# Kernel optimization log

Hardware: AMD Instinct MI355X
Metric: run time of the kernel (lower is better)

The kernel has to match this reference:

```python
import jax, jax.numpy as jnp
import numpy as np

B, L, V, E, H, DOUT = 32, 128, 30000, 300, 512, 5
NUM_STEPS = 5
WINDOW = 1


def setup_inputs() -> dict:
    key = jax.random.key(0)
    ks = jax.random.split(key, 16)
    def p(k, shape, scale=0.02):
        return jax.random.normal(k, shape, jnp.float32) * scale
    tokens = jax.random.randint(ks[0], (B, L), 1, V)
    lengths = jnp.maximum(jax.random.randint(ks[1], (B,), 1, L + 1), 8)
    embed = p(ks[2], (V, E), 0.1).at[0].set(0.0)  # padding_idx=0 row zeroed
    W0 = p(ks[3], (E, H)); b0 = jnp.zeros((H,), jnp.float32)
    Wg = p(ks[4], (3 * H + E + H, 7 * H)); bg = jnp.zeros((7 * H,), jnp.float32)
    Wgf = p(ks[5], (2 * H, H)); bgf = jnp.zeros((H,), jnp.float32)
    Wfi = p(ks[6], (2 * H, H)); bfi = jnp.zeros((H,), jnp.float32)
    Wgo = p(ks[7], (2 * H, H)); bgo = jnp.zeros((H,), jnp.float32)
    W1 = p(ks[8], (H, 2 * H)); b1 = jnp.zeros((2 * H,), jnp.float32)
    W2 = p(ks[9], (2 * H, DOUT)); b2 = jnp.zeros((DOUT,), jnp.float32)
    return dict(tokens=tokens, lengths=lengths, embed=embed, W0=W0, b0=b0,
                Wg=Wg, bg=bg, Wgf=Wgf, bgf=bgf, Wfi=Wfi, bfi=bfi,
                Wgo=Wgo, bgo=bgo, W1=W1, b1=b1, W2=W2, b2=b2)


def _shift_r(a, k):  # h_{i-k}
    return jnp.pad(a, ((0, 0), (k, 0), (0, 0)))[:, :L]


def _shift_l(a, k):  # h_{i+k}
    return jnp.pad(a, ((0, 0), (0, k), (0, 0)))[:, k:]


def reference(tokens, lengths, embed, W0, b0, Wg, bg, Wgf, bgf, Wfi, bfi,
              Wgo, bgo, W1, b1, W2, b2):
    x = embed[tokens]                                   # [B,L,E]
    mask = (jnp.arange(L)[None, :] < lengths[:, None]).astype(x.dtype)[:, :, None]
    lens = jnp.maximum(lengths.astype(x.dtype), 1.0)[:, None]  # [B,1]
    h = jnp.tanh(x @ W0 + b0) * mask                    # word node init [B,L,H]
    c = jnp.zeros_like(h)
    g = jnp.sum(h, axis=1) / lens                       # global node [B,H]
    cg = jnp.zeros_like(g)

    def step(carry, _):
        h, c, g, cg = carry
        hl = sum(_shift_r(h, k) for k in range(1, WINDOW + 1))
        hr = sum(_shift_l(h, k) for k in range(1, WINDOW + 1))
        gb = jnp.broadcast_to(g[:, None, :], h.shape)
        ctx = jnp.concatenate([hl, h, hr, x, gb], axis=-1)  # [B,L,3H+E+H]
        gates = ctx @ Wg + bg                               # [B,L,7H]
        gi, gl, gf, gr, gs, go, gu = jnp.split(gates, 7, axis=-1)
        nrm = jax.nn.softmax(jnp.stack([gi, gl, gf, gr, gs], 0), axis=0)
        i_, l_, f_, r_, s_ = nrm[0], nrm[1], nrm[2], nrm[3], nrm[4]
        o = jax.nn.sigmoid(go)
        u = jnp.tanh(gu)
        c_new = (l_ * _shift_r(c, 1) + f_ * c + r_ * _shift_l(c, 1)
                 + s_ * cg[:, None, :] + i_ * u) * mask
        h_new = o * jnp.tanh(c_new) * mask
        # global (sentence-state) node update
        h_avg = jnp.sum(h_new, axis=1) / lens
        gcat = jnp.concatenate([g, h_avg], axis=-1)         # [B,2H]
        fg = gcat @ Wgf + bgf                               # [B,H]
        og = jax.nn.sigmoid(gcat @ Wgo + bgo)
        fi = jnp.concatenate([jnp.broadcast_to(g[:, None, :], h_new.shape),
                              h_new], axis=-1) @ Wfi + bfi  # [B,L,H]
        slot_logits = jnp.concatenate([fg[:, None, :], fi], axis=1)  # [B,L+1,H]
        slot_mask = jnp.concatenate([jnp.ones((B, 1, 1), x.dtype), mask], axis=1)
        slot_logits = jnp.where(slot_mask > 0, slot_logits, -1e9)
        w = jax.nn.softmax(slot_logits, axis=1)
        cg_new = w[:, 0] * cg + jnp.sum(w[:, 1:] * c_new, axis=1)
        g_new = og * jnp.tanh(cg_new)
        return (h_new, c_new, g_new, cg_new), None

    (h, c, g, cg), _ = jax.lax.scan(step, (h, c, g, cg), None, length=NUM_STEPS)
    logits = jnp.tanh(g @ W1 + b1) @ W2 + b2            # [B,DOUT]
    return jax.nn.log_softmax(logits, axis=-1)
```

## Files before the change

### kernel.cpp

```cpp
#include <hip/hip_runtime.h>
#include <hip/hip_bf16.h>
#include <math.h>

#define B_ 32
#define L_ 128
#define LP 130
#define E_ 300
#define EP 320
#define H_ 512
#define DOUT_ 5
#define NSTEP 5
#define G7 3584
#define KGATES 1856
#define KFI 512

typedef __hip_bfloat16 bf16;
using bf16x8 = __attribute__((ext_vector_type(8))) __bf16;
using f32x4 = __attribute__((ext_vector_type(4))) float;

__device__ __forceinline__ void gload16(const void* g, void* l) {
  __builtin_amdgcn_global_load_lds(
      (const __attribute__((address_space(1))) void*)g,
      (__attribute__((address_space(3))) void*)l, 16, 0, 0);
}

__global__ void fill_zero(float* __restrict__ p, int n) {
  int i = blockIdx.x * blockDim.x + threadIdx.x;
  if (i < n) p[i] = 0.f;
}

__global__ void mask_lens_kernel(const int* __restrict__ lengths,
                                 float* __restrict__ maskf,
                                 float* __restrict__ invlens) {
  int i = blockIdx.x * blockDim.x + threadIdx.x;
  if (i < B_ * L_) {
    int b = i >> 7, l = i & 127;
    maskf[i] = (l < lengths[b]) ? 1.f : 0.f;
    if (l == 0) invlens[b] = 1.f / fmaxf((float)lengths[b], 1.f);
  }
}

__global__ void embed_bf16_kernel(const int* __restrict__ tokens,
                                  const float* __restrict__ embed,
                                  bf16* __restrict__ xb) {
  int i = blockIdx.x * blockDim.x + threadIdx.x;
  if (i >= B_ * L_ * EP) return;
  int e = i % EP, bl = i / EP;
  float v = (e < E_) ? embed[(size_t)tokens[bl] * E_ + e] : 0.f;
  xb[i] = __float2bfloat16(v);
}

__global__ void fill_pad2(bf16* __restrict__ hpad0, bf16* __restrict__ hpad1) {
  int i = blockIdx.x * blockDim.x + threadIdx.x;
  if (i >= B_ * 2 * H_) return;
  int hh = i & (H_ - 1);
  int r = (i >> 9) & 1, b = i >> 10;
  size_t oi = ((size_t)(b * LP + r * (LP - 1))) * H_ + hh;
  hpad0[oi] = __float2bfloat16(0.f);
  hpad1[oi] = __float2bfloat16(0.f);
}

__global__ __launch_bounds__(256) void transpose_to_bf16(
    const float* __restrict__ W, bf16* __restrict__ Wt, int Kreal, int Ncols,
    int dstStride) {
  __shared__ float tile[64][65];
  const int k0 = blockIdx.x * 64, n0 = blockIdx.y * 64;
  const int t = threadIdx.x;
  const int nn = t & 63, kk0 = t >> 6;
#pragma unroll
  for (int p = 0; p < 16; ++p) {
    int kk = kk0 + p * 4;
    int gk = k0 + kk;
    tile[kk][nn] = (gk < Kreal) ? W[(size_t)gk * Ncols + n0 + nn] : 0.f;
  }
  __syncthreads();
#pragma unroll
  for (int p = 0; p < 2; ++p) {
    int r = (t >> 3) + p * 32;
    int kb = (t & 7) * 8;
    union { ushort h[8]; uint4 v; } u;
#pragma unroll
    for (int e = 0; e < 8; ++e) {
      bf16 b = __float2bfloat16(tile[kb + e][r]);
      u.h[e] = *(ushort*)&b;
    }
    *(uint4*)&Wt[(size_t)(n0 + r) * dstStride + k0 + kb] = u.v;
  }
}

__global__ __launch_bounds__(256) void gemm_mfma_init(
    const bf16* __restrict__ A, const bf16* __restrict__ Bt,
    const float* __restrict__ bias, const float* __restrict__ rowscale,
    bf16* __restrict__ Cout, int N, int KP) {
  __shared__ ushort As[128 * 64];
  __shared__ ushort Bs[128 * 64];
  const int tid = threadIdx.x;
  const int lane = tid & 63;
  const int w = tid >> 6;
  const int wr = w >> 1, wc = w & 1;
  const int nbx = gridDim.x;
  const int nwg = nbx * gridDim.y;
  int id = blockIdx.y * nbx + blockIdx.x;
  if ((nwg & 7) == 0) { int q = nwg >> 3; id = (id & 7) * q + (id >> 3); }
  const int bxi = id % nbx, byi = id / nbx;
  const int rowBase = byi * 128, colBase = bxi * 128;
  const int l15 = lane & 15, l4 = lane >> 4;
  f32x4 acc[4][4] = {};

  const bf16* bP[4];
  const bf16* aP[4];
#pragma unroll
  for (int i = 0; i < 4; ++i) {
    int c = tid + 256 * i;
    int r = c >> 3;
    int ql = (c & 7) ^ (r & 7);
    bP[i] = Bt + (size_t)(colBase + r) * KP + ql * 8;
    aP[i] = A + (size_t)(rowBase + r) * KP + ql * 8;
  }

  const int nIter = KP >> 6;
  for (int t = 0; t < nIter; ++t) {
    int k0 = t * 64;
#pragma unroll
    for (int i = 0; i < 4; ++i) {
      gload16(aP[i] + k0, &As[(tid + 256 * i) * 8]);
      gload16(bP[i] + k0, &Bs[(tid + 256 * i) * 8]);
    }
    __syncthreads();
#pragma unroll
    for (int kh = 0; kh < 2; ++kh) {
      bf16x8 aF[4], bF[4];
#pragma unroll
      for (int m = 0; m < 4; ++m) {
        int row = wr * 64 + m * 16 + l15;
        aF[m] = *(const bf16x8*)&As[row * 64 +
                                    (((kh << 2) + l4) ^ (l15 & 7)) * 8];
      }
#pragma unroll
      for (int n = 0; n < 4; ++n) {
        int row = wc * 64 + n * 16 + l15;
        bF[n] = *(const bf16x8*)&Bs[row * 64 +
                                    (((kh << 2) + l4) ^ (l15 & 7)) * 8];
      }
#pragma unroll
      for (int m = 0; m < 4; ++m)
#pragma unroll
        for (int n = 0; n < 4; ++n)
          acc[m][n] = __builtin_amdgcn_mfma_f32_16x16x32_bf16(
              aF[m], bF[n], acc[m][n], 0, 0, 0);
    }
    __syncthreads();
  }

#pragma unroll
  for (int m = 0; m < 4; ++m) {
#pragma unroll
    for (int n = 0; n < 4; ++n) {
      int col = colBase + wc * 64 + n * 16 + l15;
      float bv = bias[col];
#pragma unroll
      for (int j = 0; j < 4; ++j) {
        int row = rowBase + wr * 64 + m * 16 + l4 * 4 + j;
        float v = tanhf(acc[m][n][j] + bv) * rowscale[row];
        size_t oi = ((size_t)((row >> 7) * LP + (row & 127) + 1)) * H_ + col;
        Cout[oi] = __float2bfloat16(v);
      }
    }
  }
}

__global__ __launch_bounds__(256) void gates_cell_kernel(
    const bf16* __restrict__ hpad_old, const bf16* __restrict__ xb,
    const bf16* __restrict__ Wgt, const float* __restrict__ bg,
    const float* __restrict__ gg, const int* __restrict__ lengths,
    const bf16* __restrict__ c_old, const float* __restrict__ cg_old,
    bf16* __restrict__ c_new, bf16* __restrict__ hpad_new,
    float* __restrict__ havg_part) {
  __shared__ __align__(16) char smem[64 * 113 * 4 + 16 * 16 * 4];
  ushort* As = (ushort*)smem;
  ushort* Bs = As + 64 * 64;
  float* sfi = (float*)smem;
  float* red = sfi + 64 * 113;

  const int tid = threadIdx.x;
  const int lane = tid & 63;
  const int w = tid >> 6;
  int worig = blockIdx.y * 32 + blockIdx.x;
  int id = (worig & 7) * 256 + (worig >> 3);
  const int bxi = id >> 6;
  const int byi = id & 63;
  const int b = byi >> 1, lhalf = byi & 1;
  const int len = lengths[b];
  if (lhalf && len <= 64) return;
  const int l15 = lane & 15, l4 = lane >> 4;
  f32x4 acc[7] = {};

  const int hRowBase = b * LP + lhalf * 64;
  const int blBase = b * L_ + lhalf * 64;
  const bf16* aP[2];
  const bf16* xP[2];
  const bf16* bP[4];
#pragma unroll
  for (int i = 0; i < 2; ++i) {
    int c = tid + 256 * i;
    int r = c >> 3;
    int ql = (c & 7) ^ (r & 7);
    aP[i] = hpad_old + (size_t)(hRowBase + r) * H_ + ql * 8;
    xP[i] = xb + (size_t)(blBase + r) * EP + ql * 8;
  }
#pragma unroll
  for (int i = 0; i < 4; ++i) {
    int c = tid + 256 * i;
    int r = (c < 896) ? (c >> 3) : 0;
    int ql = (c & 7) ^ (r & 7);
    int j = bxi * 112 + r;
    int src = (j % 7) * 512 + (j / 7);
    bP[i] = Wgt + (size_t)src * KGATES + ql * 8;
  }

  auto step_ = [&](const bf16* const* ap, int ko, int kb) {
#pragma unroll
    for (int i = 0; i < 2; ++i)
      gload16(ap[i] + ko, &As[(tid + 256 * i) * 8]);
#pragma unroll
    for (int i = 0; i < 3; ++i)
      gload16(bP[i] + kb, &Bs[(tid + 256 * i) * 8]);
    if (tid < 128) gload16(bP[3] + kb, &Bs[(tid + 768) * 8]);
    __syncthreads();
#pragma unroll
    for (int kh = 0; kh < 2; ++kh) {
      int arow = w * 16 + l15;
      bf16x8 aF = *(const bf16x8*)&As[arow * 64 +
                                      (((kh << 2) + l4) ^ (l15 & 7)) * 8];
      bf16x8 bF[7];
#pragma unroll
      for (int n = 0; n < 7; ++n) {
        int brow = n * 16 + l15;
        bF[n] = *(const bf16x8*)&Bs[brow * 64 +
                                    (((kh << 2) + l4) ^ (l15 & 7)) * 8];
      }
#pragma unroll
      for (int n = 0; n < 7; ++n)
        acc[n] = __builtin_amdgcn_mfma_f32_16x16x32_bf16(aF, bF[n], acc[n],
                                                         0, 0, 0);
    }
    __syncthreads();
  };

  for (int t = 0; t < 24; ++t) step_(aP, t * 64, t * 64);
  for (int t = 24; t < 29; ++t) step_(xP, (t - 24) * 64, t * 64);

#pragma unroll
  for (int n = 0; n < 7; ++n)
#pragma unroll
    for (int j = 0; j < 4; ++j)
      sfi[(w * 16 + l4 * 4 + j) * 113 + n * 16 + l15] = acc[n][j];
  __syncthreads();

  const int hloc = tid & 15;
  const int lgrp = tid >> 4;
  const int hglob = bxi * 16 + hloc;
  float bv[7];
#pragma unroll
  for (int g = 0; g < 7; ++g)
    bv[g] = bg[g * 512 + hglob] + gg[(size_t)b * G7 + g * 512 + hglob];
  const float cgv = cg_old[b * H_ + hglob];
  float s = 0.f;
#pragma unroll
  for (int it = 0; it < 4; ++it) {
    int loc = lgrp + it * 16;
    int lglob = lhalf * 64 + loc;
    int bl = b * L_ + lglob;
    size_t coi = (size_t)bl * H_ + hglob;
    size_t hoi = ((size_t)(b * LP + lglob + 1)) * H_ + hglob;
    if (lglob >= len) {
      c_new[coi] = __float2bfloat16(0.f);
      hpad_new[hoi] = __float2bfloat16(0.f);
      continue;
    }
    float gl_[7];
#pragma unroll
    for (int g = 0; g < 7; ++g) gl_[g] = sfi[loc * 113 + hloc * 7 + g] + bv[g];
    float m = fmaxf(fmaxf(fmaxf(gl_[0], gl_[1]), fmaxf(gl_[2], gl_[3])),
                    gl_[4]);
    float ei = expf(gl_[0] - m), el = expf(gl_[1] - m), ef = expf(gl_[2] - m),
          er = expf(gl_[3] - m), es = expf(gl_[4] - m);
    float inv = 1.f / (ei + el + ef + er + es);
    float o = 1.f / (1.f + expf(-gl_[5]));
    float u = tanhf(gl_[6]);
    float cprev = (lglob >= 1)
                      ? __bfloat162float(c_old[coi - H_]) : 0.f;
    float ccur = __bfloat162float(c_old[coi]);
    float cnext = (lglob < L_ - 1)
                      ? __bfloat162float(c_old[coi + H_]) : 0.f;
    float cn = (el * cprev + ef * ccur + er * cnext + es * cgv + ei * u) * inv;
    float hn = o * tanhf(cn);
    c_new[coi] = __float2bfloat16(cn);
    hpad_new[hoi] = __float2bfloat16(hn);
    s += hn;
  }
  red[hloc * 16 + lgrp] = s;
  __syncthreads();
  if (tid < 16) {
    float v = 0.f;
#pragma unroll
    for (int k = 0; k < 16; ++k) v += red[tid * 16 + k];
    havg_part[(size_t)lhalf * B_ * H_ + (size_t)b * H_ + bxi * 16 + tid] = v;
  }
}

__global__ __launch_bounds__(256) void gvec_gemm(
    const float* __restrict__ g, const float* __restrict__ Wgg,
    const float* __restrict__ Wfi, float* __restrict__ gg,
    float* __restrict__ gfi) {
  __shared__ float vin[H_];
  __shared__ float red[4][64];
  const int b = blockIdx.y;
  for (int i = threadIdx.x; i < H_; i += 256) vin[i] = g[(size_t)b * H_ + i];
  __syncthreads();
  const int o = threadIdx.x & 63, kp = threadIdx.x >> 6;
  const bool isg = blockIdx.x < 56;
  const int n0 = isg ? blockIdx.x * 64 : (blockIdx.x - 56) * 64;
  const float* W = isg ? Wgg : Wfi;
  const int ldw = isg ? G7 : H_;
  float acc = 0.f;
#pragma unroll 4
  for (int k = kp * 128; k < kp * 128 + 128; ++k)
    acc = fmaf(vin[k], W[(size_t)k * ldw + n0 + o], acc);
  red[kp][o] = acc;
  __syncthreads();
  if (threadIdx.x < 64) {
    int t = threadIdx.x;
    float v = red[0][t] + red[1][t] + red[2][t] + red[3][t];
    if (isg) gg[(size_t)b * G7 + n0 + t] = v;
    else gfi[(size_t)b * H_ + n0 + t] = v;
  }
}

__global__ __launch_bounds__(256) void gnode_vec(
    const float* __restrict__ g, const float* __restrict__ havg_part,
    const float* __restrict__ invlens, const float* __restrict__ Wgf,
    const float* __restrict__ bgf, float* __restrict__ fg,
    const float* __restrict__ Wgo, const float* __restrict__ bgo,
    float* __restrict__ og) {
  const int z = blockIdx.z;
  const float* W = z ? Wgo : Wgf;
  const float* bias = z ? bgo : bgf;
  float* op = z ? og : fg;
  __shared__ float vin[1024];
  __shared__ float red[4][64];
  const int n0 = blockIdx.x * 64, b = blockIdx.y;
  const float il = invlens[b];
  for (int i = threadIdx.x; i < 1024; i += 256)
    vin[i] = (i < 512) ? g[(size_t)b * H_ + i]
                       : (havg_part[(size_t)b * H_ + (i - 512)] +
                          havg_part[(size_t)(B_ + b) * H_ + (i - 512)]) * il;
  __syncthreads();
  const int o = threadIdx.x & 63, kp = threadIdx.x >> 6;
  float acc = 0.f;
#pragma unroll 4
  for (int k = kp * 256; k < kp * 256 + 256; ++k)
    acc = fmaf(vin[k], W[(size_t)k * H_ + n0 + o], acc);
  red[kp][o] = acc;
  __syncthreads();
  if (threadIdx.x < 64) {
    int t = threadIdx.x;
    float v = red[0][t] + red[1][t] + red[2][t] + red[3][t] + bias[n0 + t];
    if (z) v = 1.f / (1.f + expf(-v));
    op[(size_t)b * H_ + n0 + t] = v;
  }
}

__global__ __launch_bounds__(256) void fi_slot_kernel(
    const bf16* __restrict__ hpad, const bf16* __restrict__ Wfit,
    const float* __restrict__ bfi, const float* __restrict__ gfi,
    const float* __restrict__ fg, const float* __restrict__ og,
    const bf16* __restrict__ c_new, const float* __restrict__ cg_old,
    const float* __restrict__ maskf, const int* __restrict__ lengths,
    float* __restrict__ cg_new, float* __restrict__ g_new) {
  __shared__ __align__(16) char smem[64 * 129 * 4 + 3072];
  ushort* As = (ushort*)smem;
  ushort* Bs = As + 128 * 64;
  float* sfi = (float*)smem;
  float* part = sfi + 64 * 129;

  const int tid = threadIdx.x;
  const int lane = tid & 63;
  const int w = tid >> 6;
  const int b = blockIdx.y;
  const int len = lengths[b];
  const bool wactive = len > w * 32;
  const int colBase = blockIdx.x * 64;
  const int l15 = lane & 15, l4 = lane >> 4;
  f32x4 acc[2][4] = {};

  const bf16* aP[4];
  const bf16* bP[2];
#pragma unroll
  for (int i = 0; i < 4; ++i) {
    int c = tid + 256 * i;
    int r = c >> 3;
    int ql = (c & 7) ^ (r & 7);
    aP[i] = hpad + ((size_t)(b * LP + r + 1)) * H_ + ql * 8;
  }
#pragma unroll
  for (int i = 0; i < 2; ++i) {
    int c = tid + 256 * i;
    int r = c >> 3;
    int ql = (c & 7) ^ (r & 7);
    bP[i] = Wfit + (size_t)(colBase + r) * KFI + ql * 8;
  }

  for (int t = 0; t < 8; ++t) {
    int k0 = t * 64;
#pragma unroll
    for (int i = 0; i < 4; ++i)
      gload16(aP[i] + k0, &As[(tid + 256 * i) * 8]);
#pragma unroll
    for (int i = 0; i < 2; ++i)
      gload16(bP[i] + k0, &Bs[(tid + 256 * i) * 8]);
    __syncthreads();
    if (wactive) {
#pragma unroll
      for (int kh = 0; kh < 2; ++kh) {
        bf16x8 aF[2], bF[4];
#pragma unroll
        for (int m = 0; m < 2; ++m) {
          int row = w * 32 + m * 16 + l15;
          aF[m] = *(const bf16x8*)&As[row * 64 +
                                      (((kh << 2) + l4) ^ (l15 & 7)) * 8];
        }
#pragma unroll
        for (int n = 0; n < 4; ++n) {
          int row = n * 16 + l15;
          bF[n] = *(const bf16x8*)&Bs[row * 64 +
                                      (((kh << 2) + l4) ^ (l15 & 7)) * 8];
        }
#pragma unroll
        for (int m = 0; m < 2; ++m)
#pragma unroll
          for (int n = 0; n < 4; ++n)
            acc[m][n] = __builtin_amdgcn_mfma_f32_16x16x32_bf16(
                aF[m], bF[n], acc[m][n], 0, 0, 0);
      }
    }
    __syncthreads();
  }

  if (wactive) {
#pragma unroll
    for (int m = 0; m < 2; ++m) {
#pragma unroll
      for (int n = 0; n < 4; ++n) {
        int hl_ = n * 16 + l15;
        float bv = bfi[colBase + hl_] + gfi[(size_t)b * H_ + colBase + hl_];
#pragma unroll
        for (int j = 0; j < 4; ++j) {
          int l = w * 32 + m * 16 + l4 * 4 + j;
          sfi[hl_ * 129 + l] = acc[m][n][j] + bv;
        }
      }
    }
  }
  __syncthreads();

  {
    int h = tid & 63, q = tid >> 6;
    int hcol = colBase + h;
    const float* mp = maskf + b * L_;
    float m = -3.0e38f, s = 0.f, tv = 0.f;
    if (len > q * 32) {
      for (int l = q * 32; l < q * 32 + 32; ++l) {
        if (mp[l] > 0.f) {
          float xv = sfi[h * 129 + l];
          float vv =
              __bfloat162float(c_new[((size_t)(b * L_ + l)) * H_ + hcol]);
          float m2 = fmaxf(m, xv);
          float sc = expf(m - m2);
          float e = expf(xv - m2);
          s = s * sc + e;
          tv = tv * sc + e * vv;
          m = m2;
        }
      }
    }
    part[q * 192 + h] = m;
    part[q * 192 + 64 + h] = s;
    part[q * 192 + 128 + h] = tv;
  }
  __syncthreads();
  if (tid < 64) {
    int hcol = colBase + tid;
    int i0 = b * H_ + hcol;
    float mm = part[tid], s0 = part[64 + tid], t0 = part[128 + tid];
#pragma unroll
    for (int k = 1; k < 4; ++k) {
      float mk = part[k * 192 + tid];
      float m2 = fmaxf(mm, mk);
      float e1 = expf(mm - m2), e2 = expf(mk - m2);
      s0 = s0 * e1 + part[k * 192 + 64 + tid] * e2;
      t0 = t0 * e1 + part[k * 192 + 128 + tid] * e2;
      mm = m2;
    }
    float f = fg[i0];
    float m2 = fmaxf(mm, f);
    float ea = expf(mm - m2), eb = expf(f - m2);
    s0 = s0 * ea + eb;
    t0 = t0 * ea + cg_old[i0] * eb;
    float cgn = t0 / s0;
    float gn = og[i0] * tanhf(cgn);
    cg_new[i0] = cgn;
    g_new[i0] = gn;
  }
}

__global__ __launch_bounds__(256) void reduce_mean_v2(
    const bf16* __restrict__ hpad, const float* __restrict__ invlens,
    float* __restrict__ outf) {
  __shared__ float sm[4][64];
  int b = blockIdx.y, h0 = blockIdx.x * 64;
  int lg = threadIdx.x >> 6, hh = threadIdx.x & 63;
  float s = 0.f;
  for (int l = lg * 32; l < lg * 32 + 32; ++l)
    s += __bfloat162float(hpad[((size_t)(b * LP + l + 1)) * H_ + h0 + hh]);
  sm[lg][hh] = s;
  __syncthreads();
  if (threadIdx.x < 64) {
    int t = threadIdx.x;
    outf[b * H_ + h0 + t] =
        (sm[0][t] + sm[1][t] + sm[2][t] + sm[3][t]) * invlens[b];
  }
}

__global__ __launch_bounds__(256) void final_head_kernel(
    const float* __restrict__ g, const float* __restrict__ W1,
    const float* __restrict__ b1, const float* __restrict__ W2,
    const float* __restrict__ b2, float* __restrict__ out) {
  __shared__ float gv[H_];
  __shared__ float t1s[2 * H_];
  __shared__ float red[256][6];
  const int b = blockIdx.x;
  const int tid = threadIdx.x;
  for (int i = tid; i < H_; i += 256) gv[i] = g[b * H_ + i];
  __syncthreads();
  float accp[4];
#pragma unroll
  for (int p = 0; p < 4; ++p) accp[p] = b1[tid + p * 256];
  for (int k = 0; k < H_; ++k) {
    float gk = gv[k];
#pragma unroll
    for (int p = 0; p < 4; ++p)
      accp[p] = fmaf(gk, W1[(size_t)k * (2 * H_) + tid + p * 256], accp[p]);
  }
#pragma unroll
  for (int p = 0; p < 4; ++p) t1s[tid + p * 256] = tanhf(accp[p]);
  __syncthreads();
  float pd[DOUT_] = {0.f, 0.f, 0.f, 0.f, 0.f};
#pragma unroll
  for (int p = 0; p < 4; ++p) {
    int j = tid + p * 256;
    float tv = t1s[j];
#pragma unroll
    for (int d = 0; d < DOUT_; ++d)
      pd[d] = fmaf(tv, W2[(size_t)j * DOUT_ + d], pd[d]);
  }
#pragma unroll
  for (int d = 0; d < DOUT_; ++d) red[tid][d] = pd[d];
  __syncthreads();
  for (int stride = 128; stride >= 1; stride >>= 1) {
    if (tid < stride) {
#pragma unroll
      for (int d = 0; d < DOUT_; ++d) red[tid][d] += red[tid + stride][d];
    }
    __syncthreads();
  }
  if (tid == 0) {
    float lg[DOUT_];
#pragma unroll
    for (int d = 0; d < DOUT_; ++d) lg[d] = red[0][d] + b2[d];
    float m = lg[0];
#pragma unroll
    for (int d = 1; d < DOUT_; ++d) m = fmaxf(m, lg[d]);
    float s = 0.f;
#pragma unroll
    for (int d = 0; d < DOUT_; ++d) s += expf(lg[d] - m);
    float ls = logf(s);
#pragma unroll
    for (int d = 0; d < DOUT_; ++d) out[b * DOUT_ + d] = lg[d] - m - ls;
  }
}

extern "C" void kernel_launch(void* const* d_in, const int* in_sizes, int n_in,
                              void* d_out, int out_size, void* d_ws,
                              size_t ws_size, hipStream_t stream) {
  (void)in_sizes; (void)n_in; (void)out_size; (void)ws_size;
  const int* tokens = (const int*)d_in[0];
  const int* lengths = (const int*)d_in[1];
  const float* embed = (const float*)d_in[2];
  const float* W0 = (const float*)d_in[3];
  const float* b0 = (const float*)d_in[4];
  const float* Wg = (const float*)d_in[5];
  const float* bg = (const float*)d_in[6];
  const float* Wgf = (const float*)d_in[7];
  const float* bgf = (const float*)d_in[8];
  const float* Wfi = (const float*)d_in[9];
  const float* bfi = (const float*)d_in[10];
  const float* Wgo = (const float*)d_in[11];
  const float* bgo = (const float*)d_in[12];
  const float* W1 = (const float*)d_in[13];
  const float* b1 = (const float*)d_in[14];
  const float* W2 = (const float*)d_in[15];
  const float* b2 = (const float*)d_in[16];
  float* out = (float*)d_out;

  float* ws = (float*)d_ws;
  size_t off = 0;
  auto alloc = [&](size_t nf) {
    float* p = ws + off;
    off += (nf + 7) & ~(size_t)7;
    return p;
  };
  bf16* xb = (bf16*)alloc((size_t)B_ * L_ * EP / 2);
  float* maskf = alloc(B_ * L_);
  float* invlens = alloc(B_);
  bf16* hpad0 = (bf16*)alloc((size_t)B_ * LP * H_ / 2);
  bf16* hpad1 = (bf16*)alloc((size_t)B_ * LP * H_ / 2);
  bf16* cb0 = (bf16*)alloc((size_t)B_ * L_ * H_ / 2);
  bf16* cb1 = (bf16*)alloc((size_t)B_ * L_ * H_ / 2);
  float* g = alloc(B_ * H_);
  float* cgb0 = alloc(B_ * H_);
  float* cgb1 = alloc(B_ * H_);
  float* havg_part = alloc((size_t)2 * B_ * H_);
  float* fg = alloc(B_ * H_);
  float* og = alloc(B_ * H_);
  float* gg = alloc((size_t)B_ * G7);
  float* gfi = alloc(B_ * H_);
  bf16* Wgt = (bf16*)alloc((size_t)G7 * KGATES / 2);
  bf16* W0t = (bf16*)alloc((size_t)H_ * EP / 2);
  bf16* Wfit = (bf16*)alloc((size_t)H_ * KFI / 2);

  mask_lens_kernel<<<(B_ * L_ + 255) / 256, 256, 0, stream>>>(lengths, maskf,
                                                              invlens);
  embed_bf16_kernel<<<(B_ * L_ * EP + 255) / 256, 256, 0, stream>>>(tokens,
                                                                    embed, xb);
  transpose_to_bf16<<<dim3(24, G7 / 64), 256, 0, stream>>>(Wg, Wgt, 1536, G7,
                                                           KGATES);
  transpose_to_bf16<<<dim3(5, G7 / 64), 256, 0, stream>>>(
      Wg + (size_t)1536 * G7, Wgt + 1536, 300, G7, KGATES);
  transpose_to_bf16<<<dim3(5, H_ / 64), 256, 0, stream>>>(W0, W0t, 300, H_, EP);
  transpose_to_bf16<<<dim3(8, H_ / 64), 256, 0, stream>>>(
      Wfi + (size_t)H_ * H_, Wfit, H_, H_, KFI);
  fill_pad2<<<(B_ * 2 * H_ + 255) / 256, 256, 0, stream>>>(hpad0, hpad1);
  gemm_mfma_init<<<dim3(H_ / 128, (B_ * L_) / 128), 256, 0, stream>>>(
      xb, W0t, b0, maskf, hpad0, H_, EP);
  reduce_mean_v2<<<dim3(8, B_), 256, 0, stream>>>(hpad0, invlens, g);
  fill_zero<<<(B_ * L_ * H_ / 2 + 255) / 256, 256, 0, stream>>>(
      (float*)cb0, B_ * L_ * H_ / 2);
  fill_zero<<<(B_ * H_ + 255) / 256, 256, 0, stream>>>(cgb0, B_ * H_);
  fill_zero<<<(B_ * H_ + 255) / 256, 256, 0, stream>>>(havg_part + B_ * H_,
                                                       B_ * H_);

  bf16* cb[2] = {cb0, cb1};
  bf16* hp[2] = {hpad0, hpad1};
  float* cgb[2] = {cgb0, cgb1};
  int cur = 0;
  for (int step = 0; step < NSTEP; ++step) {
    int nxt = cur ^ 1;
    gvec_gemm<<<dim3(64, B_), 256, 0, stream>>>(g, Wg + (size_t)1836 * G7,
                                                Wfi, gg, gfi);
    gates_cell_kernel<<<dim3(32, 64), 256, 0, stream>>>(
        hp[cur], xb, Wgt, bg, gg, lengths, cb[cur], cgb[cur], cb[nxt],
        hp[nxt], havg_part);
    gnode_vec<<<dim3(8, B_, 2), 256, 0, stream>>>(
        g, havg_part, invlens, Wgf, bgf, fg, Wgo, bgo, og);
    fi_slot_kernel<<<dim3(8, B_), 256, 0, stream>>>(
        hp[nxt], Wfit, bfi, gfi, fg, og, cb[nxt], cgb[cur], maskf, lengths,
        cgb[nxt], g);
    cur = nxt;
  }
  final_head_kernel<<<B_, 256, 0, stream>>>(g, W1, b1, W2, b2, out);
}
```

Measured before the change: 708.6 us.

## Use split-K across waves with 128-wide K tiles in gates GEMM

```diff
diff --git a/kernel.cpp b/kernel.cpp
--- a/kernel.cpp
+++ b/kernel.cpp
@@ -6,12 +6,12 @@
 #define L_ 128
 #define LP 130
 #define E_ 300
-#define EP 320
+#define EP 384
 #define H_ 512
 #define DOUT_ 5
 #define NSTEP 5
 #define G7 3584
-#define KGATES 1856
+#define KGATES 1920
 #define KFI 512
 
 typedef __hip_bfloat16 bf16;
@@ -176,11 +176,11 @@
     const bf16* __restrict__ c_old, const float* __restrict__ cg_old,
     bf16* __restrict__ c_new, bf16* __restrict__ hpad_new,
     float* __restrict__ havg_part) {
-  __shared__ __align__(16) char smem[64 * 113 * 4 + 16 * 16 * 4];
+  __shared__ __align__(16) char smem[(64 + 112) * 128 * 2];
   ushort* As = (ushort*)smem;
-  ushort* Bs = As + 64 * 64;
+  ushort* Bs = As + 64 * 128;
   float* sfi = (float*)smem;
-  float* red = sfi + 64 * 113;
+  float* red = sfi + 112 * 68;
 
   const int tid = threadIdx.x;
   const int lane = tid & 63;
@@ -193,69 +193,87 @@
   const int len = lengths[b];
   if (lhalf && len <= 64) return;
   const int l15 = lane & 15, l4 = lane >> 4;
-  f32x4 acc[7] = {};
+  f32x4 acc[4][7] = {};
 
   const int hRowBase = b * LP + lhalf * 64;
   const int blBase = b * L_ + lhalf * 64;
-  const bf16* aP[2];
-  const bf16* xP[2];
-  const bf16* bP[4];
-#pragma unroll
-  for (int i = 0; i < 2; ++i) {
+  const bf16* aP[4];
+  const bf16* xP[4];
+  const bf16* bP[7];
+  bool aOk[4];
+#pragma unroll
+  for (int i = 0; i < 4; ++i) {
     int c = tid + 256 * i;
-    int r = c >> 3;
-    int ql = (c & 7) ^ (r & 7);
+    int r = c >> 4;
+    int ql = (c & 15) ^ (r & 7);
     aP[i] = hpad_old + (size_t)(hRowBase + r) * H_ + ql * 8;
     xP[i] = xb + (size_t)(blBase + r) * EP + ql * 8;
-  }
-#pragma unroll
-  for (int i = 0; i < 4; ++i) {
+    aOk[i] = (lhalf * 64 + r) < len;
+  }
+#pragma unroll
+  for (int i = 0; i < 7; ++i) {
     int c = tid + 256 * i;
-    int r = (c < 896) ? (c >> 3) : 0;
-    int ql = (c & 7) ^ (r & 7);
+    int r = c >> 4;
+    int ql = (c & 15) ^ (r & 7);
     int j = bxi * 112 + r;
     int src = (j % 7) * 512 + (j / 7);
     bP[i] = Wgt + (size_t)src * KGATES + ql * 8;
   }
 
+  const int kc = w * 4;
+
   auto step_ = [&](const bf16* const* ap, int ko, int kb) {
 #pragma unroll
-    for (int i = 0; i < 2; ++i)
-      gload16(ap[i] + ko, &As[(tid + 256 * i) * 8]);
-#pragma unroll
-    for (int i = 0; i < 3; ++i)
+    for (int i = 0; i < 4; ++i)
+      if (aOk[i]) gload16(ap[i] + ko, &As[(tid + 256 * i) * 8]);
+#pragma unroll
+    for (int i = 0; i < 7; ++i)
       gload16(bP[i] + kb, &Bs[(tid + 256 * i) * 8]);
-    if (tid < 128) gload16(bP[3] + kb, &Bs[(tid + 768) * 8]);
     __syncthreads();
-#pragma unroll
-    for (int kh = 0; kh < 2; ++kh) {
-      int arow = w * 16 + l15;
-      bf16x8 aF = *(const bf16x8*)&As[arow * 64 +
-                                      (((kh << 2) + l4) ^ (l15 & 7)) * 8];
-      bf16x8 bF[7];
-#pragma unroll
-      for (int n = 0; n < 7; ++n) {
-        int brow = n * 16 + l15;
-        bF[n] = *(const bf16x8*)&Bs[brow * 64 +
-                                    (((kh << 2) + l4) ^ (l15 & 7)) * 8];
-      }
+    bf16x8 aF[4], bF[7];
+#pragma unroll
+    for (int m = 0; m < 4; ++m) {
+      int row = m * 16 + l15;
+      aF[m] = *(const bf16x8*)&As[row * 128 + ((kc + l4) ^ (row & 7)) * 8];
+    }
+#pragma unroll
+    for (int n = 0; n < 7; ++n) {
+      int row = n * 16 + l15;
+      bF[n] = *(const bf16x8*)&Bs[row * 128 + ((kc + l4) ^ (row & 7)) * 8];
+    }
+#pragma unroll
+    for (int m = 0; m < 4; ++m)
 #pragma unroll
       for (int n = 0; n < 7; ++n)
-        acc[n] = __builtin_amdgcn_mfma_f32_16x16x32_bf16(aF, bF[n], acc[n],
-                                                         0, 0, 0);
-    }
+        acc[m][n] = __builtin_amdgcn_mfma_f32_16x16x32_bf16(aF[m], bF[n],
+                                                            acc[m][n], 0, 0, 0);
     __syncthreads();
   };
 
-  for (int t = 0; t < 24; ++t) step_(aP, t * 64, t * 64);
-  for (int t = 24; t < 29; ++t) step_(xP, (t - 24) * 64, t * 64);
-
-#pragma unroll
-  for (int n = 0; n < 7; ++n)
-#pragma unroll
-    for (int j = 0; j < 4; ++j)
-      sfi[(w * 16 + l4 * 4 + j) * 113 + n * 16 + l15] = acc[n][j];
-  __syncthreads();
+  for (int t = 0; t < 12; ++t) step_(aP, t * 128, t * 128);
+  for (int t = 12; t < 15; ++t) step_(xP, (t - 12) * 128, t * 128);
+
+#pragma unroll
+  for (int ww = 0; ww < 4; ++ww) {
+    if (w == ww) {
+#pragma unroll
+      for (int m = 0; m < 4; ++m)
+#pragma unroll
+        for (int n = 0; n < 7; ++n) {
+          int col = n * 16 + l15;
+          int row0 = m * 16 + l4 * 4;
+          float* dst = &sfi[col * 68 + row0];
+          if (ww == 0) {
+            *(f32x4*)dst = acc[m][n];
+          } else {
+            f32x4 v = *(const f32x4*)dst;
+            v += acc[m][n];
+            *(f32x4*)dst = v;
+          }
+        }
+    }
+    __syncthreads();
+  }
 
   const int hloc = tid & 15;
   const int lgrp = tid >> 4;
@@ -280,7 +298,8 @@
     }
     float gl_[7];
 #pragma unroll
-    for (int g = 0; g < 7; ++g) gl_[g] = sfi[loc * 113 + hloc * 7 + g] + bv[g];
+    for (int g = 0; g < 7; ++g)
+      gl_[g] = sfi[(hloc * 7 + g) * 68 + loc] + bv[g];
     float m = fmaxf(fmaxf(fmaxf(gl_[0], gl_[1]), fmaxf(gl_[2], gl_[3])),
                     gl_[4]);
     float ei = expf(gl_[0] - m), el = expf(gl_[1] - m), ef = expf(gl_[2] - m),
@@ -288,11 +307,9 @@
     float inv = 1.f / (ei + el + ef + er + es);
     float o = 1.f / (1.f + expf(-gl_[5]));
     float u = tanhf(gl_[6]);
-    float cprev = (lglob >= 1)
-                      ? __bfloat162float(c_old[coi - H_]) : 0.f;
+    float cprev = (lglob >= 1) ? __bfloat162float(c_old[coi - H_]) : 0.f;
     float ccur = __bfloat162float(c_old[coi]);
-    float cnext = (lglob < L_ - 1)
-                      ? __bfloat162float(c_old[coi + H_]) : 0.f;
+    float cnext = (lglob < L_ - 1) ? __bfloat162float(c_old[coi + H_]) : 0.f;
     float cn = (el * cprev + ef * ccur + er * cnext + es * cgv + ei * u) * inv;
     float hn = o * tanhf(cn);
     c_new[coi] = __float2bfloat16(cn);
@@ -395,6 +412,7 @@
   f32x4 acc[2][4] = {};
 
   const bf16* aP[4];
+  bool aOk[4];
   const bf16* bP[2];
 #pragma unroll
   for (int i = 0; i < 4; ++i) {
@@ -402,6 +420,7 @@
     int r = c >> 3;
     int ql = (c & 7) ^ (r & 7);
     aP[i] = hpad + ((size_t)(b * LP + r + 1)) * H_ + ql * 8;
+    aOk[i] = r < len;
   }
 #pragma unroll
   for (int i = 0; i < 2; ++i) {
@@ -415,7 +434,7 @@
     int k0 = t * 64;
 #pragma unroll
     for (int i = 0; i < 4; ++i)
-      gload16(aP[i] + k0, &As[(tid + 256 * i) * 8]);
+      if (aOk[i]) gload16(aP[i] + k0, &As[(tid + 256 * i) * 8]);
 #pragma unroll
     for (int i = 0; i < 2; ++i)
       gload16(bP[i] + k0, &Bs[(tid + 256 * i) * 8]);
@@ -645,9 +664,9 @@
                                                                     embed, xb);
   transpose_to_bf16<<<dim3(24, G7 / 64), 256, 0, stream>>>(Wg, Wgt, 1536, G7,
                                                            KGATES);
-  transpose_to_bf16<<<dim3(5, G7 / 64), 256, 0, stream>>>(
+  transpose_to_bf16<<<dim3(6, G7 / 64), 256, 0, stream>>>(
       Wg + (size_t)1536 * G7, Wgt + 1536, 300, G7, KGATES);
-  transpose_to_bf16<<<dim3(5, H_ / 64), 256, 0, stream>>>(W0, W0t, 300, H_, EP);
+  transpose_to_bf16<<<dim3(6, H_ / 64), 256, 0, stream>>>(W0, W0t, 300, H_, EP);
   transpose_to_bf16<<<dim3(8, H_ / 64), 256, 0, stream>>>(
       Wfi + (size_t)H_ * H_, Wfit, H_, H_, KFI);
   fill_pad2<<<(B_ * 2 * H_ + 255) / 256, 256, 0, stream>>>(hpad0, hpad1);
```

Result: slower. 1.173 ms (+65.5%).

## Process full sequences per gates block and skip loads for padded rows

Applied to the files above, without the earlier changes.

```diff
diff --git a/kernel.cpp b/kernel.cpp
--- a/kernel.cpp
+++ b/kernel.cpp
@@ -176,37 +176,38 @@
     const bf16* __restrict__ c_old, const float* __restrict__ cg_old,
     bf16* __restrict__ c_new, bf16* __restrict__ hpad_new,
     float* __restrict__ havg_part) {
-  __shared__ __align__(16) char smem[64 * 113 * 4 + 16 * 16 * 4];
+  __shared__ __align__(16) char smem[31488];
   ushort* As = (ushort*)smem;
-  ushort* Bs = As + 64 * 64;
+  ushort* Bs = As + 128 * 64;
   float* sfi = (float*)smem;
-  float* red = sfi + 64 * 113;
+  float* red = sfi + 112 * 68;
 
   const int tid = threadIdx.x;
   const int lane = tid & 63;
   const int w = tid >> 6;
   int worig = blockIdx.y * 32 + blockIdx.x;
-  int id = (worig & 7) * 256 + (worig >> 3);
-  const int bxi = id >> 6;
-  const int byi = id & 63;
-  const int b = byi >> 1, lhalf = byi & 1;
+  int id = (worig & 7) * 128 + (worig >> 3);
+  const int bxi = id >> 5;
+  const int b = id & 31;
   const int len = lengths[b];
-  if (lhalf && len <= 64) return;
+  const bool wok = (w * 32) < len;
   const int l15 = lane & 15, l4 = lane >> 4;
-  f32x4 acc[7] = {};
-
-  const int hRowBase = b * LP + lhalf * 64;
-  const int blBase = b * L_ + lhalf * 64;
-  const bf16* aP[2];
-  const bf16* xP[2];
+  f32x4 acc[2][7] = {};
+
+  const int hRowBase = b * LP;
+  const int blBase = b * L_;
+  const bf16* aP[4];
+  const bf16* xP[4];
   const bf16* bP[4];
-#pragma unroll
-  for (int i = 0; i < 2; ++i) {
+  bool aOk[4];
+#pragma unroll
+  for (int i = 0; i < 4; ++i) {
     int c = tid + 256 * i;
     int r = c >> 3;
     int ql = (c & 7) ^ (r & 7);
     aP[i] = hpad_old + (size_t)(hRowBase + r) * H_ + ql * 8;
     xP[i] = xb + (size_t)(blBase + r) * EP + ql * 8;
+    aOk[i] = r < len;
   }
 #pragma unroll
   for (int i = 0; i < 4; ++i) {
@@ -220,42 +221,42 @@
 
   auto step_ = [&](const bf16* const* ap, int ko, int kb) {
 #pragma unroll
-    for (int i = 0; i < 2; ++i)
-      gload16(ap[i] + ko, &As[(tid + 256 * i) * 8]);
+    for (int i = 0; i < 4; ++i)
+      if (aOk[i]) gload16(ap[i] + ko, &As[(tid + 256 * i) * 8]);
 #pragma unroll
     for (int i = 0; i < 3; ++i)
       gload16(bP[i] + kb, &Bs[(tid + 256 * i) * 8]);
     if (tid < 128) gload16(bP[3] + kb, &Bs[(tid + 768) * 8]);
     __syncthreads();
-#pragma unroll
-    for (int kh = 0; kh < 2; ++kh) {
-      int arow = w * 16 + l15;
-      bf16x8 aF = *(const bf16x8*)&As[arow * 64 +
+    if (wok) {
+#pragma unroll
+      for (int kh = 0; kh < 2; ++kh) {
+        bf16x8 aF[2], bF[7];
+#pragma unroll
+        for (int m = 0; m < 2; ++m) {
+          int row = w * 32 + m * 16 + l15;
+          aF[m] = *(const bf16x8*)&As[row * 64 +
                                       (((kh << 2) + l4) ^ (l15 & 7)) * 8];
-      bf16x8 bF[7];
-#pragma unroll
-      for (int n = 0; n < 7; ++n) {
-        int brow = n * 16 + l15;
-        bF[n] = *(const bf16x8*)&Bs[brow * 64 +
-                                    (((kh << 2) + l4) ^ (l15 & 7)) * 8];
+        }
+#pragma unroll
+        for (int n = 0; n < 7; ++n) {
+          int row = n * 16 + l15;
+          bF[n] = *(const bf16x8*)&Bs[row * 64 +
+                                      (((kh << 2) + l4) ^ (l15 & 7)) * 8];
+        }
+#pragma unroll
+        for (int m = 0; m < 2; ++m)
+#pragma unroll
+          for (int n = 0; n < 7; ++n)
+            acc[m][n] = __builtin_amdgcn_mfma_f32_16x16x32_bf16(
+                aF[m], bF[n], acc[m][n], 0, 0, 0);
       }
-#pragma unroll
-      for (int n = 0; n < 7; ++n)
-        acc[n] = __builtin_amdgcn_mfma_f32_16x16x32_bf16(aF, bF[n], acc[n],
-                                                         0, 0, 0);
     }
     __syncthreads();
   };
 
   for (int t = 0; t < 24; ++t) step_(aP, t * 64, t * 64);
   for (int t = 24; t < 29; ++t) step_(xP, (t - 24) * 64, t * 64);
-
-#pragma unroll
-  for (int n = 0; n < 7; ++n)
-#pragma unroll
-    for (int j = 0; j < 4; ++j)
-      sfi[(w * 16 + l4 * 4 + j) * 113 + n * 16 + l15] = acc[n][j];
-  __syncthreads();
 
   const int hloc = tid & 15;
   const int lgrp = tid >> 4;
@@ -267,37 +268,54 @@
   const float cgv = cg_old[b * H_ + hglob];
   float s = 0.f;
 #pragma unroll
-  for (int it = 0; it < 4; ++it) {
-    int loc = lgrp + it * 16;
-    int lglob = lhalf * 64 + loc;
-    int bl = b * L_ + lglob;
-    size_t coi = (size_t)bl * H_ + hglob;
-    size_t hoi = ((size_t)(b * LP + lglob + 1)) * H_ + hglob;
-    if (lglob >= len) {
-      c_new[coi] = __float2bfloat16(0.f);
-      hpad_new[hoi] = __float2bfloat16(0.f);
-      continue;
-    }
-    float gl_[7];
-#pragma unroll
-    for (int g = 0; g < 7; ++g) gl_[g] = sfi[loc * 113 + hloc * 7 + g] + bv[g];
-    float m = fmaxf(fmaxf(fmaxf(gl_[0], gl_[1]), fmaxf(gl_[2], gl_[3])),
-                    gl_[4]);
-    float ei = expf(gl_[0] - m), el = expf(gl_[1] - m), ef = expf(gl_[2] - m),
-          er = expf(gl_[3] - m), es = expf(gl_[4] - m);
-    float inv = 1.f / (ei + el + ef + er + es);
-    float o = 1.f / (1.f + expf(-gl_[5]));
-    float u = tanhf(gl_[6]);
-    float cprev = (lglob >= 1)
-                      ? __bfloat162float(c_old[coi - H_]) : 0.f;
-    float ccur = __bfloat162float(c_old[coi]);
-    float cnext = (lglob < L_ - 1)
-                      ? __bfloat162float(c_old[coi + H_]) : 0.f;
-    float cn = (el * cprev + ef * ccur + er * cnext + es * cgv + ei * u) * inv;
-    float hn = o * tanhf(cn);
-    c_new[coi] = __float2bfloat16(cn);
-    hpad_new[hoi] = __float2bfloat16(hn);
-    s += hn;
+  for (int p = 0; p < 2; ++p) {
+    if ((w >> 1) == p && wok) {
+      const int wloc = w & 1;
+#pragma unroll
+      for (int m = 0; m < 2; ++m)
+#pragma unroll
+        for (int n = 0; n < 7; ++n) {
+          int col = n * 16 + l15;
+          int row0 = wloc * 32 + m * 16 + l4 * 4;
+          *(f32x4*)&sfi[col * 68 + row0] = acc[m][n];
+        }
+    }
+    __syncthreads();
+#pragma unroll
+    for (int it = 0; it < 4; ++it) {
+      int loc = lgrp + it * 16;
+      int lglob = p * 64 + loc;
+      int bl = b * L_ + lglob;
+      size_t coi = (size_t)bl * H_ + hglob;
+      size_t hoi = ((size_t)(b * LP + lglob + 1)) * H_ + hglob;
+      if (lglob >= len) {
+        c_new[coi] = __float2bfloat16(0.f);
+        hpad_new[hoi] = __float2bfloat16(0.f);
+        continue;
+      }
+      float gl_[7];
+#pragma unroll
+      for (int g = 0; g < 7; ++g)
+        gl_[g] = sfi[(hloc * 7 + g) * 68 + loc] + bv[g];
+      float m = fmaxf(fmaxf(fmaxf(gl_[0], gl_[1]), fmaxf(gl_[2], gl_[3])),
+                      gl_[4]);
+      float ei = expf(gl_[0] - m), el = expf(gl_[1] - m),
+            ef = expf(gl_[2] - m), er = expf(gl_[3] - m),
+            es = expf(gl_[4] - m);
+      float inv = 1.f / (ei + el + ef + er + es);
+      float o = 1.f / (1.f + expf(-gl_[5]));
+      float u = tanhf(gl_[6]);
+      float cprev = (lglob >= 1) ? __bfloat162float(c_old[coi - H_]) : 0.f;
+      float ccur = __bfloat162float(c_old[coi]);
+      float cnext = (lglob < L_ - 1) ? __bfloat162float(c_old[coi + H_]) : 0.f;
+      float cn =
+          (el * cprev + ef * ccur + er * cnext + es * cgv + ei * u) * inv;
+      float hn = o * tanhf(cn);
+      c_new[coi] = __float2bfloat16(cn);
+      hpad_new[hoi] = __float2bfloat16(hn);
+      s += hn;
+    }
+    __syncthreads();
   }
   red[hloc * 16 + lgrp] = s;
   __syncthreads();
@@ -305,7 +323,7 @@
     float v = 0.f;
 #pragma unroll
     for (int k = 0; k < 16; ++k) v += red[tid * 16 + k];
-    havg_part[(size_t)lhalf * B_ * H_ + (size_t)b * H_ + bxi * 16 + tid] = v;
+    havg_part[(size_t)b * H_ + bxi * 16 + tid] = v;
   }
 }
 
@@ -395,6 +413,7 @@
   f32x4 acc[2][4] = {};
 
   const bf16* aP[4];
+  bool aOk[4];
   const bf16* bP[2];
 #pragma unroll
   for (int i = 0; i < 4; ++i) {
@@ -402,6 +421,7 @@
     int r = c >> 3;
     int ql = (c & 7) ^ (r & 7);
     aP[i] = hpad + ((size_t)(b * LP + r + 1)) * H_ + ql * 8;
+    aOk[i] = r < len;
   }
 #pragma unroll
   for (int i = 0; i < 2; ++i) {
@@ -415,7 +435,7 @@
     int k0 = t * 64;
 #pragma unroll
     for (int i = 0; i < 4; ++i)
-      gload16(aP[i] + k0, &As[(tid + 256 * i) * 8]);
+      if (aOk[i]) gload16(aP[i] + k0, &As[(tid + 256 * i) * 8]);
 #pragma unroll
     for (int i = 0; i < 2; ++i)
       gload16(bP[i] + k0, &Bs[(tid + 256 * i) * 8]);
@@ -668,7 +688,7 @@
     int nxt = cur ^ 1;
     gvec_gemm<<<dim3(64, B_), 256, 0, stream>>>(g, Wg + (size_t)1836 * G7,
                                                 Wfi, gg, gfi);
-    gates_cell_kernel<<<dim3(32, 64), 256, 0, stream>>>(
+    gates_cell_kernel<<<dim3(32, 32), 256, 0, stream>>>(
         hp[cur], xb, Wgt, bg, gg, lengths, cb[cur], cgb[cur], cb[nxt],
         hp[nxt], havg_part);
     gnode_vec<<<dim3(8, B_, 2), 256, 0, stream>>>(
```

Measured after the change: 676.5 us. -4.5%, faster.
